# Performance work log

Hardware: AMD Instinct MI355X
Metric: run time of the kernel (lower is better)

## Reference

```python
import jax, jax.numpy as jnp
import numpy as np

N_ATOMS = 200000
N_CHANNELS = 4
N_EDGES = 12800000
PREFACTOR = 1.0


def setup_inputs() -> dict:
    key = jax.random.key(0)
    k1, k2, k3, k4, k5 = jax.random.split(key, 5)
    charges = jax.random.normal(k1, (N_ATOMS, N_CHANNELS), dtype=jnp.float32)
    cell = jax.random.normal(k2, (3, 3), dtype=jnp.float32)
    positions = jax.random.normal(k3, (N_ATOMS, 3), dtype=jnp.float32)
    neighbor_indices = jax.random.randint(k4, (N_EDGES, 2), 0, N_ATOMS, dtype=jnp.int32)
    # distances in (0.5, 5.5) to keep 1/r well-conditioned
    neighbor_distances = jax.random.uniform(k5, (N_EDGES,), dtype=jnp.float32,
                                            minval=0.5, maxval=5.5)
    return {
        "charges": charges,
        "cell": cell,
        "positions": positions,
        "neighbor_indices": neighbor_indices,
        "neighbor_distances": neighbor_distances,
    }


def reference(charges, cell, positions, neighbor_indices, neighbor_distances):
    # Potential.from_dist for a Coulomb potential with smearing=None: v(r) = 1/r
    potentials_bare = 1.0 / neighbor_distances  # [n_edges]
    atom_is = neighbor_indices[:, 0]
    atom_js = neighbor_indices[:, 1]
    # gather charge of neighbor j, weight by pair potential, scatter-add into atom i
    contributions_is = charges[atom_js] * potentials_bare[:, None]  # [n_edges, n_channels]
    potential = jnp.zeros_like(charges).at[atom_is].add(contributions_is)
    # half neighbor list (full_neighbor_list=False): symmetric term into atom j
    contributions_js = charges[atom_is] * potentials_bare[:, None]
    potential = potential.at[atom_js].add(contributions_js)
    return PREFACTOR * (potential * 0.5)  # [n_atoms, n_channels]
```

## Files before the change

kernel.cpp:

```cpp
#include <hip/hip_runtime.h>


#define BLOCK   256
#define NBLK    512
#define AB_LOG  11
#define A_B     2048
#define MAXNB   128
#define NSLICE  4

static __device__ __forceinline__ unsigned long long nt_u64(const void* p) {
    return __builtin_nontemporal_load((const unsigned long long*)p);
}
static __device__ __forceinline__ float nt_f32(const float* p) {
    return __builtin_nontemporal_load(p);
}

__global__ __launch_bounds__(BLOCK) void k_hist(
    const int2* __restrict__ nbr, int* __restrict__ blk_hist,
    int n_edges, int nb)
{
    __shared__ int h[MAXNB];
    for (int i = threadIdx.x; i < nb; i += blockDim.x) h[i] = 0;
    __syncthreads();
    int per = (n_edges + gridDim.x - 1) / gridDim.x;
    int lo = blockIdx.x * per;
    int hi = min(lo + per, n_edges);
    for (int e = lo + threadIdx.x; e < hi; e += blockDim.x) {
        int2 ij = nbr[e];
        atomicAdd(&h[ij.x >> AB_LOG], 1);
        atomicAdd(&h[ij.y >> AB_LOG], 1);
    }
    __syncthreads();
    for (int i = threadIdx.x; i < nb; i += blockDim.x)
        blk_hist[i * NBLK + blockIdx.x] = h[i];
}

__global__ __launch_bounds__(NBLK) void k_rowscan(
    const int* __restrict__ blk_hist, int* __restrict__ offs,
    int* __restrict__ totals)
{
    __shared__ int a[NBLK];
    int b = blockIdx.x, t = threadIdx.x;
    int v = blk_hist[b * NBLK + t];
    a[t] = v;
    __syncthreads();
    for (int off = 1; off < NBLK; off <<= 1) {
        int x = (t >= off) ? a[t - off] : 0;
        __syncthreads();
        a[t] += x;
        __syncthreads();
    }
    offs[b * NBLK + t] = a[t] - v;
    if (t == NBLK - 1) totals[b] = a[t];
}

__global__ void k_bases(const int* __restrict__ totals, int* __restrict__ bases, int nb)
{
    if (threadIdx.x == 0) {
        int s = 0;
        for (int b = 0; b < nb; ++b) { bases[b] = s; s += totals[b]; }
    }
}

__global__ void k_addbase(int* __restrict__ offs, const int* __restrict__ bases, int n)
{
    int i = blockIdx.x * blockDim.x + threadIdx.x;
    if (i < n) offs[i] += bases[i >> 9];
}

__global__ __launch_bounds__(BLOCK) void k_scatter(
    const int2* __restrict__ nbr, const float* __restrict__ dist,
    const int* __restrict__ offs, uint2* __restrict__ tuples,
    int n_edges, int nb)
{
    __shared__ int cur[MAXNB];
    for (int i = threadIdx.x; i < nb; i += blockDim.x)
        cur[i] = offs[i * NBLK + blockIdx.x];
    __syncthreads();
    int per = (n_edges + gridDim.x - 1) / gridDim.x;
    int lo = blockIdx.x * per;
    int hi = min(lo + per, n_edges);
    for (int e = lo + threadIdx.x; e < hi; e += blockDim.x) {
        unsigned long long v = nt_u64(&nbr[e]);
        int ix = (int)(v & 0xffffffffu);
        int iy = (int)(v >> 32);
        float w = 0.5f / nt_f32(&dist[e]);
        unsigned wb = __float_as_uint(w);
        int pi = atomicAdd(&cur[ix >> AB_LOG], 1);
        tuples[pi] = make_uint2((unsigned)(ix & (A_B - 1)) | ((unsigned)iy << AB_LOG), wb);
        int pj = atomicAdd(&cur[iy >> AB_LOG], 1);
        tuples[pj] = make_uint2((unsigned)(iy & (A_B - 1)) | ((unsigned)ix << AB_LOG), wb);
    }
}

__global__ __launch_bounds__(BLOCK) void k_accum(
    const uint2* __restrict__ tuples, const float4* __restrict__ charges,
    const int* __restrict__ bases, const int* __restrict__ totals,
    float* __restrict__ partials)
{
    __shared__ float acc[A_B * 4];
    int b = blockIdx.x >> 2;
    int s = blockIdx.x & 3;
    for (int i = threadIdx.x; i < A_B * 4; i += blockDim.x) acc[i] = 0.f;
    __syncthreads();
    int start = bases[b], cnt = totals[b];
    int lo = start + cnt * s / NSLICE;
    int hi = start + cnt * (s + 1) / NSLICE;
    for (int p = lo + threadIdx.x; p < hi; p += blockDim.x) {
        unsigned long long v = nt_u64(&tuples[p]);
        unsigned packed = (unsigned)(v & 0xffffffffu);
        float w = __uint_as_float((unsigned)(v >> 32));
        int dest = packed & (A_B - 1);
        int src  = packed >> AB_LOG;
        float4 c = charges[src];
        atomicAdd(&acc[dest * 4 + 0], c.x * w);
        atomicAdd(&acc[dest * 4 + 1], c.y * w);
        atomicAdd(&acc[dest * 4 + 2], c.z * w);
        atomicAdd(&acc[dest * 4 + 3], c.w * w);
    }
    __syncthreads();
    float* outp = partials + (size_t)blockIdx.x * (A_B * 4);
    for (int i = threadIdx.x; i < A_B * 4; i += blockDim.x) outp[i] = acc[i];
}

__global__ void k_final(const float4* __restrict__ partials,
                        float4* __restrict__ out, int n_atoms)
{
    int a = blockIdx.x * blockDim.x + threadIdx.x;
    if (a >= n_atoms) return;
    int b = a >> AB_LOG;
    int local = a & (A_B - 1);
    const float4* p = partials + (size_t)(b * NSLICE) * A_B + local;
    float4 s0 = p[0], s1 = p[A_B], s2 = p[2 * A_B], s3 = p[3 * A_B];
    float4 r;
    r.x = s0.x + s1.x + s2.x + s3.x;
    r.y = s0.y + s1.y + s2.y + s3.y;
    r.z = s0.z + s1.z + s2.z + s3.z;
    r.w = s0.w + s1.w + s2.w + s3.w;
    out[a] = r;
}

__global__ __launch_bounds__(BLOCK) void edge_scatter_agent(
    const float4* __restrict__ charges, const int2* __restrict__ nbr,
    const float* __restrict__ dist, float* __restrict__ out, int n_edges)
{
    int e = blockIdx.x * blockDim.x + threadIdx.x;
    if (e >= n_edges) return;
    int2 ij = nbr[e];
    float w = 0.5f / dist[e];
    float4 cj = charges[ij.y];
    float4 ci = charges[ij.x];
    float* oi = out + (size_t)ij.x * 4;
    float* oj = out + (size_t)ij.y * 4;
    atomicAdd(oi + 0, cj.x * w); atomicAdd(oi + 1, cj.y * w);
    atomicAdd(oi + 2, cj.z * w); atomicAdd(oi + 3, cj.w * w);
    atomicAdd(oj + 0, ci.x * w); atomicAdd(oj + 1, ci.y * w);
    atomicAdd(oj + 2, ci.z * w); atomicAdd(oj + 3, ci.w * w);
}

extern "C" void kernel_launch(void* const* d_in, const int* in_sizes, int n_in,
                              void* d_out, int out_size, void* d_ws, size_t ws_size,
                              hipStream_t stream)
{
    const float4* charges = (const float4*)d_in[0];
    const int2*   nbr     = (const int2*)d_in[3];
    const float*  dist    = (const float*)d_in[4];

    int n_edges = in_sizes[4];
    int n_atoms = out_size / 4;
    int nb = (n_atoms + A_B - 1) >> AB_LOG;

    size_t n_pairs = (size_t)2 * n_edges;
    char*  w   = (char*)d_ws;
    size_t off = 0;
    auto alloc = [&](size_t bytes) -> void* {
        void* p = w + off;
        off += (bytes + 255) & ~(size_t)255;
        return p;
    };
    uint2* tuples   = (uint2*)alloc(n_pairs * sizeof(uint2));
    int*   blk_hist = (int*)  alloc((size_t)nb * NBLK * sizeof(int));
    int*   offs     = (int*)  alloc((size_t)nb * NBLK * sizeof(int));
    int*   totals   = (int*)  alloc((size_t)nb * sizeof(int));
    int*   bases    = (int*)  alloc((size_t)nb * sizeof(int));
    float* partials = (float*)alloc((size_t)nb * NSLICE * A_B * 4 * sizeof(float));

    if (off <= ws_size && nb <= MAXNB) {
        k_hist   <<<NBLK, BLOCK, 0, stream>>>(nbr, blk_hist, n_edges, nb);
        k_rowscan<<<nb,   NBLK,  0, stream>>>(blk_hist, offs, totals);
        k_bases  <<<1,    64,    0, stream>>>(totals, bases, nb);
        k_addbase<<<(nb * NBLK + 255) / 256, 256, 0, stream>>>(offs, bases, nb * NBLK);
        k_scatter<<<NBLK, BLOCK, 0, stream>>>(nbr, dist, offs, tuples, n_edges, nb);
        k_accum  <<<nb * NSLICE, BLOCK, 0, stream>>>(tuples, charges, bases, totals, partials);
        k_final  <<<(n_atoms + 255) / 256, 256, 0, stream>>>(
            (const float4*)partials, (float4*)d_out, n_atoms);
    } else {
        hipMemsetAsync(d_out, 0, (size_t)out_size * sizeof(float), stream);
        edge_scatter_agent<<<(n_edges + BLOCK - 1) / BLOCK, BLOCK, 0, stream>>>(
            charges, nbr, dist, (float*)d_out, n_edges);
    }
}
```

Baseline: 1.043 ms.

## Shrink atom buckets, add more slices per bucket, unroll accumulation and parallelize bases scan

Atom buckets shrink from 2048 to 1024 atoms and histogram blocks double to 1024. The number of accumulation slices per bucket now adapts up to 16 based on workspace size, and the final reduction loops over however many slices were chosen. The accumulation loop is unrolled 4x to issue tuple and charge loads ahead of the LDS atomics, the histogram uses nontemporal loads, and the serial bases scan becomes a parallel block scan. This is meant to raise parallelism and occupancy in k_accum (smaller LDS footprint, far more blocks). The cost is more partial buffers to write and reduce, and larger histogram and scan arrays.

Result: no change. 1.030 ms (-1.3%).

```diff
diff --git a/kernel.cpp b/kernel.cpp
--- a/kernel.cpp
+++ b/kernel.cpp
@@ -2,11 +2,11 @@
 
 
 #define BLOCK   256
-#define NBLK    512
-#define AB_LOG  11
-#define A_B     2048
-#define MAXNB   128
-#define NSLICE  4
+#define NBLK    1024
+#define NBLK_LG 10
+#define AB_LOG  10
+#define A_B     1024
+#define MAXNB   256
 
 static __device__ __forceinline__ unsigned long long nt_u64(const void* p) {
     return __builtin_nontemporal_load((const unsigned long long*)p);
@@ -25,10 +25,13 @@
     int per = (n_edges + gridDim.x - 1) / gridDim.x;
     int lo = blockIdx.x * per;
     int hi = min(lo + per, n_edges);
+    #pragma unroll 4
     for (int e = lo + threadIdx.x; e < hi; e += blockDim.x) {
-        int2 ij = nbr[e];
-        atomicAdd(&h[ij.x >> AB_LOG], 1);
-        atomicAdd(&h[ij.y >> AB_LOG], 1);
+        unsigned long long v = nt_u64(&nbr[e]);
+        int ix = (int)(v & 0xffffffffu);
+        int iy = (int)(v >> 32);
+        atomicAdd(&h[ix >> AB_LOG], 1);
+        atomicAdd(&h[iy >> AB_LOG], 1);
     }
     __syncthreads();
     for (int i = threadIdx.x; i < nb; i += blockDim.x)
@@ -54,18 +57,27 @@
     if (t == NBLK - 1) totals[b] = a[t];
 }
 
-__global__ void k_bases(const int* __restrict__ totals, int* __restrict__ bases, int nb)
-{
-    if (threadIdx.x == 0) {
-        int s = 0;
-        for (int b = 0; b < nb; ++b) { bases[b] = s; s += totals[b]; }
-    }
+__global__ __launch_bounds__(MAXNB) void k_bases(
+    const int* __restrict__ totals, int* __restrict__ bases, int nb)
+{
+    __shared__ int a[MAXNB];
+    int t = threadIdx.x;
+    int v = (t < nb) ? totals[t] : 0;
+    a[t] = v;
+    __syncthreads();
+    for (int off = 1; off < MAXNB; off <<= 1) {
+        int x = (t >= off) ? a[t - off] : 0;
+        __syncthreads();
+        a[t] += x;
+        __syncthreads();
+    }
+    if (t < nb) bases[t] = a[t] - v;
 }
 
 __global__ void k_addbase(int* __restrict__ offs, const int* __restrict__ bases, int n)
 {
     int i = blockIdx.x * blockDim.x + threadIdx.x;
-    if (i < n) offs[i] += bases[i >> 9];
+    if (i < n) offs[i] += bases[i >> NBLK_LG];
 }
 
 __global__ __launch_bounds__(BLOCK) void k_scatter(
@@ -80,6 +92,7 @@
     int per = (n_edges + gridDim.x - 1) / gridDim.x;
     int lo = blockIdx.x * per;
     int hi = min(lo + per, n_edges);
+    #pragma unroll 2
     for (int e = lo + threadIdx.x; e < hi; e += blockDim.x) {
         unsigned long long v = nt_u64(&nbr[e]);
         int ix = (int)(v & 0xffffffffu);
@@ -96,27 +109,47 @@
 __global__ __launch_bounds__(BLOCK) void k_accum(
     const uint2* __restrict__ tuples, const float4* __restrict__ charges,
     const int* __restrict__ bases, const int* __restrict__ totals,
-    float* __restrict__ partials)
+    float* __restrict__ partials, int nslice)
 {
     __shared__ float acc[A_B * 4];
-    int b = blockIdx.x >> 2;
-    int s = blockIdx.x & 3;
+    int b = blockIdx.x / nslice;
+    int s = blockIdx.x % nslice;
     for (int i = threadIdx.x; i < A_B * 4; i += blockDim.x) acc[i] = 0.f;
     __syncthreads();
     int start = bases[b], cnt = totals[b];
-    int lo = start + cnt * s / NSLICE;
-    int hi = start + cnt * (s + 1) / NSLICE;
-    for (int p = lo + threadIdx.x; p < hi; p += blockDim.x) {
-        unsigned long long v = nt_u64(&tuples[p]);
-        unsigned packed = (unsigned)(v & 0xffffffffu);
-        float w = __uint_as_float((unsigned)(v >> 32));
-        int dest = packed & (A_B - 1);
-        int src  = packed >> AB_LOG;
-        float4 c = charges[src];
-        atomicAdd(&acc[dest * 4 + 0], c.x * w);
-        atomicAdd(&acc[dest * 4 + 1], c.y * w);
-        atomicAdd(&acc[dest * 4 + 2], c.z * w);
-        atomicAdd(&acc[dest * 4 + 3], c.w * w);
+    int lo = start + (int)((long long)cnt * s / nslice);
+    int hi = start + (int)((long long)cnt * (s + 1) / nslice);
+
+    int p = lo + threadIdx.x;
+    for (; p + 3 * BLOCK < hi; p += 4 * BLOCK) {
+        uint2 t0 = tuples[p];
+        uint2 t1 = tuples[p + BLOCK];
+        uint2 t2 = tuples[p + 2 * BLOCK];
+        uint2 t3 = tuples[p + 3 * BLOCK];
+        float4 c0 = charges[t0.x >> AB_LOG];
+        float4 c1 = charges[t1.x >> AB_LOG];
+        float4 c2 = charges[t2.x >> AB_LOG];
+        float4 c3 = charges[t3.x >> AB_LOG];
+        float w0 = __uint_as_float(t0.y), w1 = __uint_as_float(t1.y);
+        float w2 = __uint_as_float(t2.y), w3 = __uint_as_float(t3.y);
+        int d0 = (t0.x & (A_B - 1)) * 4, d1 = (t1.x & (A_B - 1)) * 4;
+        int d2 = (t2.x & (A_B - 1)) * 4, d3 = (t3.x & (A_B - 1)) * 4;
+        atomicAdd(&acc[d0 + 0], c0.x * w0); atomicAdd(&acc[d0 + 1], c0.y * w0);
+        atomicAdd(&acc[d0 + 2], c0.z * w0); atomicAdd(&acc[d0 + 3], c0.w * w0);
+        atomicAdd(&acc[d1 + 0], c1.x * w1); atomicAdd(&acc[d1 + 1], c1.y * w1);
+        atomicAdd(&acc[d1 + 2], c1.z * w1); atomicAdd(&acc[d1 + 3], c1.w * w1);
+        atomicAdd(&acc[d2 + 0], c2.x * w2); atomicAdd(&acc[d2 + 1], c2.y * w2);
+        atomicAdd(&acc[d2 + 2], c2.z * w2); atomicAdd(&acc[d2 + 3], c2.w * w2);
+        atomicAdd(&acc[d3 + 0], c3.x * w3); atomicAdd(&acc[d3 + 1], c3.y * w3);
+        atomicAdd(&acc[d3 + 2], c3.z * w3); atomicAdd(&acc[d3 + 3], c3.w * w3);
+    }
+    for (; p < hi; p += BLOCK) {
+        uint2 t = tuples[p];
+        float4 c = charges[t.x >> AB_LOG];
+        float w = __uint_as_float(t.y);
+        int d = (t.x & (A_B - 1)) * 4;
+        atomicAdd(&acc[d + 0], c.x * w); atomicAdd(&acc[d + 1], c.y * w);
+        atomicAdd(&acc[d + 2], c.z * w); atomicAdd(&acc[d + 3], c.w * w);
     }
     __syncthreads();
     float* outp = partials + (size_t)blockIdx.x * (A_B * 4);
@@ -124,19 +157,18 @@
 }
 
 __global__ void k_final(const float4* __restrict__ partials,
-                        float4* __restrict__ out, int n_atoms)
+                        float4* __restrict__ out, int n_atoms, int nslice)
 {
     int a = blockIdx.x * blockDim.x + threadIdx.x;
     if (a >= n_atoms) return;
     int b = a >> AB_LOG;
     int local = a & (A_B - 1);
-    const float4* p = partials + (size_t)(b * NSLICE) * A_B + local;
-    float4 s0 = p[0], s1 = p[A_B], s2 = p[2 * A_B], s3 = p[3 * A_B];
-    float4 r;
-    r.x = s0.x + s1.x + s2.x + s3.x;
-    r.y = s0.y + s1.y + s2.y + s3.y;
-    r.z = s0.z + s1.z + s2.z + s3.z;
-    r.w = s0.w + s1.w + s2.w + s3.w;
+    const float4* p = partials + (size_t)(b * nslice) * A_B + local;
+    float4 r = make_float4(0.f, 0.f, 0.f, 0.f);
+    for (int s = 0; s < nslice; ++s) {
+        float4 t = p[(size_t)s * A_B];
+        r.x += t.x; r.y += t.y; r.z += t.z; r.w += t.w;
+    }
     out[a] = r;
 }
 
@@ -183,17 +215,22 @@
     int*   offs     = (int*)  alloc((size_t)nb * NBLK * sizeof(int));
     int*   totals   = (int*)  alloc((size_t)nb * sizeof(int));
     int*   bases    = (int*)  alloc((size_t)nb * sizeof(int));
-    float* partials = (float*)alloc((size_t)nb * NSLICE * A_B * 4 * sizeof(float));
+
+    size_t slice_bytes = (size_t)nb * A_B * 4 * sizeof(float);
+    int nslice = 16;
+    while (nslice > 1 && off + (size_t)nslice * slice_bytes > ws_size) nslice >>= 1;
+    float* partials = (float*)alloc((size_t)nslice * slice_bytes);
 
     if (off <= ws_size && nb <= MAXNB) {
         k_hist   <<<NBLK, BLOCK, 0, stream>>>(nbr, blk_hist, n_edges, nb);
         k_rowscan<<<nb,   NBLK,  0, stream>>>(blk_hist, offs, totals);
-        k_bases  <<<1,    64,    0, stream>>>(totals, bases, nb);
+        k_bases  <<<1,    MAXNB, 0, stream>>>(totals, bases, nb);
         k_addbase<<<(nb * NBLK + 255) / 256, 256, 0, stream>>>(offs, bases, nb * NBLK);
         k_scatter<<<NBLK, BLOCK, 0, stream>>>(nbr, dist, offs, tuples, n_edges, nb);
-        k_accum  <<<nb * NSLICE, BLOCK, 0, stream>>>(tuples, charges, bases, totals, partials);
+        k_accum  <<<nb * nslice, BLOCK, 0, stream>>>(tuples, charges, bases, totals,
+                                                     partials, nslice);
         k_final  <<<(n_atoms + 255) / 256, 256, 0, stream>>>(
-            (const float4*)partials, (float4*)d_out, n_atoms);
+            (const float4*)partials, (float4*)d_out, n_atoms, nslice);
     } else {
         hipMemsetAsync(d_out, 0, (size_t)out_size * sizeof(float), stream);
         edge_scatter_agent<<<(n_edges + BLOCK - 1) / BLOCK, BLOCK, 0, stream>>>(
```

## Bucket pairs by destination and source atom tiles to stage charges in LDS

Applied to the files above, without the earlier changes.

Replaces the 1D destination-block bucketing with a 2D (destination tile, source tile) key sort. The accumulation kernel can then stage each 4096-atom source charge tile in shared memory and gather from LDS instead of doing random global charge reads. Accumulators move to a channel-planar layout, blocks change to 512 threads, loads are unrolled and partials use nontemporal stores. The cost is a larger histogram and scan (about 2500 keys times 192 blocks), more partial slices to reduce, and scatter writes spread over many more buckets, which hurts write locality.

Measured after the change: 1.519 ms. 1.46x slower.

```diff
diff --git a/kernel.cpp b/kernel.cpp
--- a/kernel.cpp
+++ b/kernel.cpp
@@ -1,12 +1,14 @@
 #include <hip/hip_runtime.h>
 
 
-#define BLOCK   256
-#define NBLK    512
-#define AB_LOG  11
-#define A_B     2048
-#define MAXNB   128
-#define NSLICE  4
+#define DB_LOG   12
+#define D_B      4096
+#define SB_LOG   12
+#define S_B      4096
+#define KEYS_MAX 2560
+#define NBLK_S   192
+#define SBLOCK   512
+#define GPB      3
 
 static __device__ __forceinline__ unsigned long long nt_u64(const void* p) {
     return __builtin_nontemporal_load((const unsigned long long*)p);
@@ -14,133 +16,216 @@
 static __device__ __forceinline__ float nt_f32(const float* p) {
     return __builtin_nontemporal_load(p);
 }
-
-__global__ __launch_bounds__(BLOCK) void k_hist(
-    const int2* __restrict__ nbr, int* __restrict__ blk_hist,
-    int n_edges, int nb)
-{
-    __shared__ int h[MAXNB];
-    for (int i = threadIdx.x; i < nb; i += blockDim.x) h[i] = 0;
+static __device__ __forceinline__ void nt_store(float* p, float v) {
+    __builtin_nontemporal_store(v, p);
+}
+
+__global__ __launch_bounds__(SBLOCK) void k_hist(
+    const int2* __restrict__ nbr, int* __restrict__ tmp,
+    int n_edges, int nkeys, int ns)
+{
+    __shared__ int h[KEYS_MAX];
+    for (int i = threadIdx.x; i < nkeys; i += blockDim.x) h[i] = 0;
     __syncthreads();
     int per = (n_edges + gridDim.x - 1) / gridDim.x;
     int lo = blockIdx.x * per;
     int hi = min(lo + per, n_edges);
+    #pragma unroll 4
     for (int e = lo + threadIdx.x; e < hi; e += blockDim.x) {
-        int2 ij = nbr[e];
-        atomicAdd(&h[ij.x >> AB_LOG], 1);
-        atomicAdd(&h[ij.y >> AB_LOG], 1);
-    }
-    __syncthreads();
-    for (int i = threadIdx.x; i < nb; i += blockDim.x)
-        blk_hist[i * NBLK + blockIdx.x] = h[i];
-}
-
-__global__ __launch_bounds__(NBLK) void k_rowscan(
-    const int* __restrict__ blk_hist, int* __restrict__ offs,
-    int* __restrict__ totals)
-{
-    __shared__ int a[NBLK];
-    int b = blockIdx.x, t = threadIdx.x;
-    int v = blk_hist[b * NBLK + t];
+        unsigned long long v = nt_u64(&nbr[e]);
+        int ix = (int)(v & 0xffffffffu);
+        int iy = (int)(v >> 32);
+        atomicAdd(&h[(ix >> DB_LOG) * ns + (iy >> SB_LOG)], 1);
+        atomicAdd(&h[(iy >> DB_LOG) * ns + (ix >> SB_LOG)], 1);
+    }
+    __syncthreads();
+    int* row = tmp + (size_t)blockIdx.x * nkeys;
+    for (int i = threadIdx.x; i < nkeys; i += blockDim.x) row[i] = h[i];
+}
+
+__global__ __launch_bounds__(256) void k_rowscan(
+    const int* __restrict__ tmp, int* __restrict__ offs,
+    int* __restrict__ totals, int nkeys)
+{
+    __shared__ int a[256];
+    int key = blockIdx.x, t = threadIdx.x;
+    int v = (t < NBLK_S) ? tmp[(size_t)t * nkeys + key] : 0;
     a[t] = v;
     __syncthreads();
-    for (int off = 1; off < NBLK; off <<= 1) {
+    for (int off = 1; off < 256; off <<= 1) {
         int x = (t >= off) ? a[t - off] : 0;
         __syncthreads();
         a[t] += x;
         __syncthreads();
     }
-    offs[b * NBLK + t] = a[t] - v;
-    if (t == NBLK - 1) totals[b] = a[t];
-}
-
-__global__ void k_bases(const int* __restrict__ totals, int* __restrict__ bases, int nb)
-{
-    if (threadIdx.x == 0) {
-        int s = 0;
-        for (int b = 0; b < nb; ++b) { bases[b] = s; s += totals[b]; }
-    }
-}
-
-__global__ void k_addbase(int* __restrict__ offs, const int* __restrict__ bases, int n)
+    if (t < NBLK_S) offs[(size_t)t * nkeys + key] = a[t] - v;
+    if (t == 255) totals[key] = a[t];
+}
+
+__global__ __launch_bounds__(1024) void k_bases(
+    const int* __restrict__ totals, int* __restrict__ key_base, int nkeys)
+{
+    __shared__ int a[1024];
+    int t = threadIdx.x;
+    int i0 = 3 * t;
+    int s0 = (i0     < nkeys) ? totals[i0]     : 0;
+    int s1 = (i0 + 1 < nkeys) ? totals[i0 + 1] : 0;
+    int s2 = (i0 + 2 < nkeys) ? totals[i0 + 2] : 0;
+    int local = s0 + s1 + s2;
+    a[t] = local;
+    __syncthreads();
+    for (int off = 1; off < 1024; off <<= 1) {
+        int x = (t >= off) ? a[t - off] : 0;
+        __syncthreads();
+        a[t] += x;
+        __syncthreads();
+    }
+    int base = a[t] - local;
+    if (i0     < nkeys) key_base[i0]     = base;
+    if (i0 + 1 < nkeys) key_base[i0 + 1] = base + s0;
+    if (i0 + 2 < nkeys) key_base[i0 + 2] = base + s0 + s1;
+}
+
+__global__ void k_addbase(int* __restrict__ offs, const int* __restrict__ key_base,
+                          int n, int nkeys)
 {
     int i = blockIdx.x * blockDim.x + threadIdx.x;
-    if (i < n) offs[i] += bases[i >> 9];
-}
-
-__global__ __launch_bounds__(BLOCK) void k_scatter(
+    if (i < n) offs[i] += key_base[i % nkeys];
+}
+
+__global__ __launch_bounds__(SBLOCK) void k_scatter(
     const int2* __restrict__ nbr, const float* __restrict__ dist,
     const int* __restrict__ offs, uint2* __restrict__ tuples,
-    int n_edges, int nb)
-{
-    __shared__ int cur[MAXNB];
-    for (int i = threadIdx.x; i < nb; i += blockDim.x)
-        cur[i] = offs[i * NBLK + blockIdx.x];
+    int n_edges, int nkeys, int ns)
+{
+    __shared__ int cur[KEYS_MAX];
+    const int* row = offs + (size_t)blockIdx.x * nkeys;
+    for (int i = threadIdx.x; i < nkeys; i += blockDim.x) cur[i] = row[i];
     __syncthreads();
     int per = (n_edges + gridDim.x - 1) / gridDim.x;
     int lo = blockIdx.x * per;
     int hi = min(lo + per, n_edges);
+    #pragma unroll 4
     for (int e = lo + threadIdx.x; e < hi; e += blockDim.x) {
         unsigned long long v = nt_u64(&nbr[e]);
         int ix = (int)(v & 0xffffffffu);
         int iy = (int)(v >> 32);
         float w = 0.5f / nt_f32(&dist[e]);
         unsigned wb = __float_as_uint(w);
-        int pi = atomicAdd(&cur[ix >> AB_LOG], 1);
-        tuples[pi] = make_uint2((unsigned)(ix & (A_B - 1)) | ((unsigned)iy << AB_LOG), wb);
-        int pj = atomicAdd(&cur[iy >> AB_LOG], 1);
-        tuples[pj] = make_uint2((unsigned)(iy & (A_B - 1)) | ((unsigned)ix << AB_LOG), wb);
-    }
-}
-
-__global__ __launch_bounds__(BLOCK) void k_accum(
+        int k1 = (ix >> DB_LOG) * ns + (iy >> SB_LOG);
+        int p1 = atomicAdd(&cur[k1], 1);
+        tuples[p1] = make_uint2((unsigned)(ix & (D_B - 1)) |
+                                ((unsigned)(iy & (S_B - 1)) << 12), wb);
+        int k2 = (iy >> DB_LOG) * ns + (ix >> SB_LOG);
+        int p2 = atomicAdd(&cur[k2], 1);
+        tuples[p2] = make_uint2((unsigned)(iy & (D_B - 1)) |
+                                ((unsigned)(ix & (S_B - 1)) << 12), wb);
+    }
+}
+
+__global__ __launch_bounds__(SBLOCK) void k_accum(
     const uint2* __restrict__ tuples, const float4* __restrict__ charges,
-    const int* __restrict__ bases, const int* __restrict__ totals,
-    float* __restrict__ partials)
-{
-    __shared__ float acc[A_B * 4];
-    int b = blockIdx.x >> 2;
-    int s = blockIdx.x & 3;
-    for (int i = threadIdx.x; i < A_B * 4; i += blockDim.x) acc[i] = 0.f;
-    __syncthreads();
-    int start = bases[b], cnt = totals[b];
-    int lo = start + cnt * s / NSLICE;
-    int hi = start + cnt * (s + 1) / NSLICE;
-    for (int p = lo + threadIdx.x; p < hi; p += blockDim.x) {
-        unsigned long long v = nt_u64(&tuples[p]);
-        unsigned packed = (unsigned)(v & 0xffffffffu);
-        float w = __uint_as_float((unsigned)(v >> 32));
-        int dest = packed & (A_B - 1);
-        int src  = packed >> AB_LOG;
-        float4 c = charges[src];
-        atomicAdd(&acc[dest * 4 + 0], c.x * w);
-        atomicAdd(&acc[dest * 4 + 1], c.y * w);
-        atomicAdd(&acc[dest * 4 + 2], c.z * w);
-        atomicAdd(&acc[dest * 4 + 3], c.w * w);
-    }
-    __syncthreads();
-    float* outp = partials + (size_t)blockIdx.x * (A_B * 4);
-    for (int i = threadIdx.x; i < A_B * 4; i += blockDim.x) outp[i] = acc[i];
-}
-
-__global__ void k_final(const float4* __restrict__ partials,
-                        float4* __restrict__ out, int n_atoms)
+    const int* __restrict__ key_base, const int* __restrict__ totals,
+    float* __restrict__ partials, int n_atoms, int ns, int slices)
+{
+    extern __shared__ char sm[];
+    float*  acc   = (float*)sm;
+    float4* stage = (float4*)(sm + 4 * D_B * sizeof(float));
+
+    int d = blockIdx.x / slices;
+    int s = blockIdx.x % slices;
+
+    for (int i = threadIdx.x; i < 4 * D_B; i += blockDim.x) acc[i] = 0.f;
+
+    int g_lo = s * GPB;
+    int g_hi = min(g_lo + GPB, ns);
+    const unsigned long long* tp = (const unsigned long long*)tuples;
+
+    for (int g = g_lo; g < g_hi; ++g) {
+        __syncthreads();
+        int base_atom = g << SB_LOG;
+        for (int i = threadIdx.x; i < S_B; i += blockDim.x) {
+            int ga = base_atom + i;
+            stage[i] = (ga < n_atoms) ? charges[ga] : make_float4(0.f, 0.f, 0.f, 0.f);
+        }
+        __syncthreads();
+
+        int key = d * ns + g;
+        int lo = key_base[key];
+        int hi = lo + totals[key];
+
+        int p = lo + threadIdx.x;
+        for (; p + 3 * SBLOCK < hi; p += 4 * SBLOCK) {
+            unsigned long long t0 = nt_u64(&tp[p]);
+            unsigned long long t1 = nt_u64(&tp[p + SBLOCK]);
+            unsigned long long t2 = nt_u64(&tp[p + 2 * SBLOCK]);
+            unsigned long long t3 = nt_u64(&tp[p + 3 * SBLOCK]);
+            unsigned u0 = (unsigned)t0, u1 = (unsigned)t1;
+            unsigned u2 = (unsigned)t2, u3 = (unsigned)t3;
+            float4 c0 = stage[(u0 >> 12) & (S_B - 1)];
+            float4 c1 = stage[(u1 >> 12) & (S_B - 1)];
+            float4 c2 = stage[(u2 >> 12) & (S_B - 1)];
+            float4 c3 = stage[(u3 >> 12) & (S_B - 1)];
+            float w0 = __uint_as_float((unsigned)(t0 >> 32));
+            float w1 = __uint_as_float((unsigned)(t1 >> 32));
+            float w2 = __uint_as_float((unsigned)(t2 >> 32));
+            float w3 = __uint_as_float((unsigned)(t3 >> 32));
+            int d0 = u0 & (D_B - 1), d1 = u1 & (D_B - 1);
+            int d2 = u2 & (D_B - 1), d3 = u3 & (D_B - 1);
+            atomicAdd(&acc[d0],             c0.x * w0);
+            atomicAdd(&acc[D_B + d0],       c0.y * w0);
+            atomicAdd(&acc[2 * D_B + d0],   c0.z * w0);
+            atomicAdd(&acc[3 * D_B + d0],   c0.w * w0);
+            atomicAdd(&acc[d1],             c1.x * w1);
+            atomicAdd(&acc[D_B + d1],       c1.y * w1);
+            atomicAdd(&acc[2 * D_B + d1],   c1.z * w1);
+            atomicAdd(&acc[3 * D_B + d1],   c1.w * w1);
+            atomicAdd(&acc[d2],             c2.x * w2);
+            atomicAdd(&acc[D_B + d2],       c2.y * w2);
+            atomicAdd(&acc[2 * D_B + d2],   c2.z * w2);
+            atomicAdd(&acc[3 * D_B + d2],   c2.w * w2);
+            atomicAdd(&acc[d3],             c3.x * w3);
+            atomicAdd(&acc[D_B + d3],       c3.y * w3);
+            atomicAdd(&acc[2 * D_B + d3],   c3.z * w3);
+            atomicAdd(&acc[3 * D_B + d3],   c3.w * w3);
+        }
+        for (; p < hi; p += SBLOCK) {
+            unsigned long long t = nt_u64(&tp[p]);
+            unsigned u = (unsigned)t;
+            float4 c = stage[(u >> 12) & (S_B - 1)];
+            float w = __uint_as_float((unsigned)(t >> 32));
+            int dd = u & (D_B - 1);
+            atomicAdd(&acc[dd],           c.x * w);
+            atomicAdd(&acc[D_B + dd],     c.y * w);
+            atomicAdd(&acc[2 * D_B + dd], c.z * w);
+            atomicAdd(&acc[3 * D_B + dd], c.w * w);
+        }
+    }
+    __syncthreads();
+    float* outp = partials + (size_t)blockIdx.x * (4 * D_B);
+    for (int i = threadIdx.x; i < 4 * D_B; i += blockDim.x)
+        nt_store(&outp[i], acc[i]);
+}
+
+__global__ void k_final(const float* __restrict__ partials,
+                        float4* __restrict__ out, int n_atoms, int slices)
 {
     int a = blockIdx.x * blockDim.x + threadIdx.x;
     if (a >= n_atoms) return;
-    int b = a >> AB_LOG;
-    int local = a & (A_B - 1);
-    const float4* p = partials + (size_t)(b * NSLICE) * A_B + local;
-    float4 s0 = p[0], s1 = p[A_B], s2 = p[2 * A_B], s3 = p[3 * A_B];
-    float4 r;
-    r.x = s0.x + s1.x + s2.x + s3.x;
-    r.y = s0.y + s1.y + s2.y + s3.y;
-    r.z = s0.z + s1.z + s2.z + s3.z;
-    r.w = s0.w + s1.w + s2.w + s3.w;
-    out[a] = r;
-}
-
-__global__ __launch_bounds__(BLOCK) void edge_scatter_agent(
+    int d = a >> DB_LOG;
+    int dl = a & (D_B - 1);
+    float r0 = 0.f, r1 = 0.f, r2 = 0.f, r3 = 0.f;
+    for (int s = 0; s < slices; ++s) {
+        const float* p = partials + (size_t)(d * slices + s) * (4 * D_B) + dl;
+        r0 += p[0];
+        r1 += p[D_B];
+        r2 += p[2 * D_B];
+        r3 += p[3 * D_B];
+    }
+    out[a] = make_float4(r0, r1, r2, r3);
+}
+
+__global__ __launch_bounds__(256) void edge_scatter_agent(
     const float4* __restrict__ charges, const int2* __restrict__ nbr,
     const float* __restrict__ dist, float* __restrict__ out, int n_edges)
 {
@@ -168,7 +253,11 @@
 
     int n_edges = in_sizes[4];
     int n_atoms = out_size / 4;
-    int nb = (n_atoms + A_B - 1) >> AB_LOG;
+    int nd = (n_atoms + D_B - 1) >> DB_LOG;
+    int ns = (n_atoms + S_B - 1) >> SB_LOG;
+    int nkeys = nd * ns;
+    int slices = (ns + GPB - 1) / GPB;
+    int nacc = nd * slices;
 
     size_t n_pairs = (size_t)2 * n_edges;
     char*  w   = (char*)d_ws;
@@ -179,24 +268,29 @@
         return p;
     };
     uint2* tuples   = (uint2*)alloc(n_pairs * sizeof(uint2));
-    int*   blk_hist = (int*)  alloc((size_t)nb * NBLK * sizeof(int));
-    int*   offs     = (int*)  alloc((size_t)nb * NBLK * sizeof(int));
-    int*   totals   = (int*)  alloc((size_t)nb * sizeof(int));
-    int*   bases    = (int*)  alloc((size_t)nb * sizeof(int));
-    float* partials = (float*)alloc((size_t)nb * NSLICE * A_B * 4 * sizeof(float));
-
-    if (off <= ws_size && nb <= MAXNB) {
-        k_hist   <<<NBLK, BLOCK, 0, stream>>>(nbr, blk_hist, n_edges, nb);
-        k_rowscan<<<nb,   NBLK,  0, stream>>>(blk_hist, offs, totals);
-        k_bases  <<<1,    64,    0, stream>>>(totals, bases, nb);
-        k_addbase<<<(nb * NBLK + 255) / 256, 256, 0, stream>>>(offs, bases, nb * NBLK);
-        k_scatter<<<NBLK, BLOCK, 0, stream>>>(nbr, dist, offs, tuples, n_edges, nb);
-        k_accum  <<<nb * NSLICE, BLOCK, 0, stream>>>(tuples, charges, bases, totals, partials);
+    int*   tmp      = (int*)  alloc((size_t)NBLK_S * nkeys * sizeof(int));
+    int*   offs     = (int*)  alloc((size_t)NBLK_S * nkeys * sizeof(int));
+    int*   totals   = (int*)  alloc((size_t)nkeys * sizeof(int));
+    int*   key_base = (int*)  alloc((size_t)nkeys * sizeof(int));
+    float* partials = (float*)alloc((size_t)nacc * 4 * D_B * sizeof(float));
+
+    size_t lds_accum = (size_t)4 * D_B * sizeof(float) + (size_t)S_B * sizeof(float4);
+
+    if (off <= ws_size && nkeys <= KEYS_MAX) {
+        k_hist   <<<NBLK_S, SBLOCK, 0, stream>>>(nbr, tmp, n_edges, nkeys, ns);
+        k_rowscan<<<nkeys,  256,    0, stream>>>(tmp, offs, totals, nkeys);
+        k_bases  <<<1,      1024,   0, stream>>>(totals, key_base, nkeys);
+        k_addbase<<<(NBLK_S * nkeys + 511) / 512, 512, 0, stream>>>(
+            offs, key_base, NBLK_S * nkeys, nkeys);
+        k_scatter<<<NBLK_S, SBLOCK, 0, stream>>>(nbr, dist, offs, tuples,
+                                                 n_edges, nkeys, ns);
+        k_accum  <<<nacc, SBLOCK, lds_accum, stream>>>(
+            tuples, charges, key_base, totals, partials, n_atoms, ns, slices);
         k_final  <<<(n_atoms + 255) / 256, 256, 0, stream>>>(
-            (const float4*)partials, (float4*)d_out, n_atoms);
+            partials, (float4*)d_out, n_atoms, slices);
     } else {
         hipMemsetAsync(d_out, 0, (size_t)out_size * sizeof(float), stream);
-        edge_scatter_agent<<<(n_edges + BLOCK - 1) / BLOCK, BLOCK, 0, stream>>>(
+        edge_scatter_agent<<<(n_edges + 255) / 256, 256, 0, stream>>>(
             charges, nbr, dist, (float*)d_out, n_edges);
     }
 }
```
